# Kernel tuning notes

Measured on AMD Instinct MI355X. Metric: run time of the kernel, lower is better.

Reference implementation:

```python
import jax, jax.numpy as jnp
import numpy as np

D_MODEL = 1024
NUM_HEADS = 16
NUM_GROUPS = 4
HEAD_DIM = D_MODEL // NUM_HEADS
ROPE_BASE = 10000.0


def _rope_tables(seq_len, head_dim, dtype=jnp.float32):
    inv_freq = 1.0 / (ROPE_BASE ** (jnp.arange(0, head_dim, 2, dtype=jnp.float32) / head_dim))
    freqs = jnp.arange(seq_len, dtype=jnp.float32)[:, None] * inv_freq[None, :]  # [S, hd/2]
    emb = jnp.concatenate([freqs, freqs], axis=-1)  # [S, hd]
    return jnp.cos(emb).astype(dtype), jnp.sin(emb).astype(dtype)


def _rotate_half(t):
    half = t.shape[-1] // 2
    return jnp.concatenate([-t[..., half:], t[..., :half]], axis=-1)


def _apply_rope(t, cos, sin):
    # t: [B,S,H,hd]; cos/sin: [S,hd] broadcast over batch and heads
    c = cos[None, :, None, :]
    s = sin[None, :, None, :]
    return t * c + _rotate_half(t) * s


def setup_inputs() -> dict:
    key = jax.random.key(0)
    ks = jax.random.split(key, 5)
    B, S, D = 2, 2048, D_MODEL
    scale = 1.0 / np.sqrt(D)
    return {
        "x": jax.random.normal(ks[0], (B, S, D), dtype=jnp.float32),
        "Wq": jax.random.normal(ks[1], (D, D), dtype=jnp.float32) * scale,
        "Wk": jax.random.normal(ks[2], (D, D), dtype=jnp.float32) * scale,
        "Wv": jax.random.normal(ks[3], (D, D), dtype=jnp.float32) * scale,
        "Wo": jax.random.normal(ks[4], (D, D), dtype=jnp.float32) * scale,
    }


def reference(x, Wq, Wk, Wv, Wo):
    B, S, D = x.shape
    H, G, hd = NUM_HEADS, NUM_GROUPS, HEAD_DIM
    hpg = H // G  # heads per group

    q = (x @ Wq.T).reshape(B, S, H, hd)
    k = (x @ Wk.T).reshape(B, S, H, hd)
    v = (x @ Wv.T).reshape(B, S, H, hd)

    cos, sin = _rope_tables(S, hd, x.dtype)
    q = _apply_rope(q, cos, sin)
    k = _apply_rope(k, cos, sin)

    # query head reordering: [B,S,G,hpg,hd] -> transpose(2,3) -> [B,S,H,hd]
    q = q.reshape(B, S, G, hpg, hd).swapaxes(2, 3).reshape(B, S, H, hd)
    # GQA group-mean of K/V, then repeat back to H heads
    k = k.reshape(B, S, G, hpg, hd).mean(axis=3)  # [B,S,G,hd]
    v = v.reshape(B, S, G, hpg, hd).mean(axis=3)
    k = jnp.repeat(k, hpg, axis=2)  # [B,S,H,hd]
    v = jnp.repeat(v, hpg, axis=2)

    q = q.transpose(0, 2, 1, 3)  # [B,H,S,hd]
    k = k.transpose(0, 2, 1, 3)
    v = v.transpose(0, 2, 1, 3)

    scores = jnp.einsum('bhqd,bhkd->bhqk', q, k) / np.sqrt(hd)  # [B,H,S,S]
    probs = jax.nn.softmax(scores, axis=-1)
    attn = jnp.einsum('bhqk,bhkd->bhqd', probs, v)

    attn = attn.transpose(0, 2, 1, 3).reshape(B, S, D)
    return attn @ Wo.T
```

## Files before the change

### kernel.cpp

```cpp
#include <hip/hip_runtime.h>
#include <hip/hip_bf16.h>
#include <math.h>

#define B_ 2
#define S_ 2048
#define D_ 1024
#define H_ 16
#define G_ 4
#define HD_ 64

typedef float f32x4  __attribute__((ext_vector_type(4)));
typedef float f32x16 __attribute__((ext_vector_type(16)));
typedef short s16x8  __attribute__((ext_vector_type(8)));
typedef unsigned short u16x4 __attribute__((ext_vector_type(4)));
typedef unsigned int   u32x4 __attribute__((ext_vector_type(4)));

__device__ __forceinline__ unsigned short f2b(float f) {
    __hip_bfloat16 h = __float2bfloat16(f);
    return __builtin_bit_cast(unsigned short, h);
}
__device__ __forceinline__ unsigned cvtpk(float lo, float hi) {
    unsigned r;
    asm("v_cvt_pk_bf16_f32 %0, %1, %2" : "=v"(r) : "v"(lo), "v"(hi));
    return r;
}
__device__ __forceinline__ void plswap(unsigned &a, unsigned &b) {
    asm("v_permlane32_swap_b32 %0, %1" : "+v"(a), "+v"(b));
}

#define MFMA16(a, b, c) __builtin_amdgcn_mfma_f32_16x16x32_bf16(a, b, c, 0, 0, 0)
#define MFMA32(a, b, c) __builtin_amdgcn_mfma_f32_32x32x16_bf16(a, b, c, 0, 0, 0)

#define GLOAD16(gp, lp) __builtin_amdgcn_global_load_lds(                      \
    (const __attribute__((address_space(1))) void*)(gp),                      \
    (__attribute__((address_space(3))) void*)(lp), 16, 0, 0)

__global__ __launch_bounds__(256)
void prep_all(const float* __restrict__ x,  const float* __restrict__ Wq,
              const float* __restrict__ Wk, const float* __restrict__ Wv,
              const float* __restrict__ Wo,
              unsigned short* __restrict__ xb, unsigned short* __restrict__ wb,
              unsigned short* __restrict__ wob,
              float* __restrict__ cost, float* __restrict__ sint)
{
    const int NQ_WB = (1536*1024)/4;
    const int NQ_WO = (1024*1024)/4;
    const int NQ_X  = (B_*S_*D_)/4;
    int q = blockIdx.x*256 + threadIdx.x;
    if (q < NQ_WB) {
        const int idx = q*4, row = idx >> 10, c = idx & 1023;
        u16x4 o;
        if (row < 1024) {
            f32x4 v = *(const f32x4*)&Wq[(size_t)row*1024 + c];
            #pragma unroll
            for (int j = 0; j < 4; ++j) o[j] = f2b(v[j]);
        } else {
            const int rd = row - 1024, kv = rd >> 8, gd = rd & 255;
            const int g = gd >> 6, d = gd & 63;
            const float* W = kv ? Wv : Wk;
            f32x4 sum = {0.f, 0.f, 0.f, 0.f};
            #pragma unroll
            for (int p = 0; p < 4; ++p)
                sum += *(const f32x4*)&W[(size_t)((g*4 + p)*64 + d)*1024 + c];
            #pragma unroll
            for (int j = 0; j < 4; ++j) o[j] = f2b(sum[j]*0.25f);
        }
        *(u16x4*)&wb[idx] = o;
        return;
    }
    q -= NQ_WB;
    if (q < NQ_WO) {
        const int idx = q*4;
        f32x4 v = *(const f32x4*)&Wo[idx];
        u16x4 o;
        #pragma unroll
        for (int j = 0; j < 4; ++j) o[j] = f2b(v[j]);
        *(u16x4*)&wob[idx] = o;
        return;
    }
    q -= NQ_WO;
    if (q < NQ_X) {
        const int idx = q*4;
        f32x4 v = *(const f32x4*)&x[idx];
        u16x4 o;
        #pragma unroll
        for (int j = 0; j < 4; ++j) o[j] = f2b(v[j]);
        *(u16x4*)&xb[idx] = o;
        return;
    }
    q -= NQ_X;
    if (q < (S_*32)/4) {
        const int idx = q*4, s = idx >> 5, f0 = idx & 31;
        #pragma unroll
        for (int j = 0; j < 4; ++j) {
            const float f = (float)(f0 + j);
            const float fr = (float)s * powf(10000.0f, -f*(1.0f/32.0f));
            cost[idx + j] = cosf(fr);
            sint[idx + j] = sinf(fr);
        }
    }
}

template<int MODE>
__global__ __launch_bounds__(256)
void gemm_mfma(const unsigned short* __restrict__ Am,
               const unsigned short* __restrict__ Bm,
               unsigned short* __restrict__ qr,
               unsigned short* __restrict__ kr,
               unsigned short* __restrict__ vt,
               float* __restrict__ outf,
               const float* __restrict__ cost,
               const float* __restrict__ sint,
               int nbx)
{
    __shared__ unsigned short As[2][64*64];
    __shared__ unsigned short Bs[2][128*64];

    const int nwg = gridDim.x;
    const int cpx = nwg >> 3;
    const int bid = blockIdx.x;
    const int swz = (bid & 7)*cpx + (bid >> 3);
    const int bx = swz % nbx, by = swz / nbx;

    const int t  = threadIdx.x;
    const int w  = t >> 6, l = t & 63;
    const int lg = l >> 4, lr = l & 15;
    const int wr = w >> 1, wc = w & 1;

    const unsigned short* gA = Am + (size_t)by*64*D_;
    const unsigned short* gB = Bm + (size_t)bx*128*D_;

    const int srow = l >> 3;
    const int schk = (l & 7) ^ srow;

#define STAGE(buf, k0)                                                         \
    _Pragma("unroll")                                                          \
    for (int i_ = 0; i_ < 2; ++i_) {                                           \
        const int rowA_ = 16*w + 8*i_ + srow;                                  \
        GLOAD16(gA + (size_t)rowA_*D_ + (k0) + 8*schk, &As[buf][(16*w + 8*i_)*64]); \
    }                                                                          \
    _Pragma("unroll")                                                          \
    for (int i_ = 0; i_ < 4; ++i_) {                                           \
        const int rowB_ = 32*w + 8*i_ + srow;                                  \
        GLOAD16(gB + (size_t)rowB_*D_ + (k0) + 8*schk, &Bs[buf][(32*w + 8*i_)*64]); \
    }

    f32x4 acc[2][4] = {};

    STAGE(0, 0);
    #pragma unroll 1
    for (int kt = 0; kt < 16; ++kt) {
        const int cur = kt & 1;
        if (kt < 15) {
            STAGE(cur ^ 1, 64*(kt + 1));
            asm volatile("s_waitcnt vmcnt(6)" ::: "memory");
        } else {
            asm volatile("s_waitcnt vmcnt(0)" ::: "memory");
        }
        __builtin_amdgcn_s_barrier();

        #pragma unroll
        for (int kk = 0; kk < 2; ++kk) {
            s16x8 af[2], bfr[4];
            #pragma unroll
            for (int m = 0; m < 2; ++m) {
                const int row = 32*wr + 16*m + lr;
                af[m] = *(const s16x8*)&As[cur][row*64 + 8*((lg + 4*kk) ^ (row & 7))];
            }
            #pragma unroll
            for (int n = 0; n < 4; ++n) {
                const int col = 64*wc + 16*n + lr;
                bfr[n] = *(const s16x8*)&Bs[cur][col*64 + 8*((lg + 4*kk) ^ (col & 7))];
            }
            #pragma unroll
            for (int m = 0; m < 2; ++m)
                #pragma unroll
                for (int n = 0; n < 4; ++n)
                    acc[m][n] = MFMA16(af[m], bfr[n], acc[m][n]);
        }
        asm volatile("s_waitcnt lgkmcnt(0)" ::: "memory");
        __builtin_amdgcn_s_barrier();
    }
#undef STAGE

    if (MODE == 1) {
        #pragma unroll
        for (int m = 0; m < 2; ++m)
            #pragma unroll
            for (int r = 0; r < 4; ++r) {
                const int row = by*64 + 32*wr + 16*m + 4*lg + r;
                #pragma unroll
                for (int n = 0; n < 4; ++n)
                    outf[(size_t)row*D_ + bx*128 + 64*wc + 16*n + lr] = acc[m][n][r];
            }
        return;
    }

    if (bx < 10) {
        const float CQ = 0.18033688011112044f;
        #pragma unroll
        for (int m = 0; m < 2; ++m) {
            #pragma unroll
            for (int r = 0; r < 4; ++r) {
                const int row = by*64 + 32*wr + 16*m + 4*lg + r;
                const int b = row >> 11, s = row & (S_ - 1);
                const float c_lo = cost[s*32 + lr],      s_lo = sint[s*32 + lr];
                const float c_hi = cost[s*32 + 16 + lr], s_hi = sint[s*32 + 16 + lr];
                unsigned short vals[4];
                #pragma unroll
                for (int n = 0; n < 4; ++n) {
                    const float cc = (n & 1) ? c_hi : c_lo;
                    const float sn = (n & 1) ? s_hi : s_lo;
                    const float self = acc[m][n][r], part = acc[m][n ^ 2][r];
                    float rv = (n < 2) ? fmaf(self, cc, -part*sn)
                                       : fmaf(self, cc,  part*sn);
                    if (bx < 8) rv *= CQ;
                    vals[n] = f2b(rv);
                }
                size_t base;
                unsigned short* dst;
                if (bx < 8) {
                    const int hh = 2*bx + wc;
                    const int hp = (hh & 3)*4 + (hh >> 2);
                    base = (((size_t)b*H_ + hp)*S_ + s)*HD_;
                    dst = qr;
                } else {
                    const int g = (bx - 8)*2 + wc;
                    base = (((size_t)b*G_ + g)*S_ + s)*HD_;
                    dst = kr;
                }
                #pragma unroll
                for (int n = 0; n < 4; ++n) dst[base + 16*n + lr] = vals[n];
            }
        }
    } else {
        const int g = (bx - 10)*2 + wc;
        #pragma unroll
        for (int m = 0; m < 2; ++m) {
            const int row0 = by*64 + 32*wr + 16*m + 4*lg;
            const int b = row0 >> 11, s0 = row0 & (S_ - 1);
            #pragma unroll
            for (int n = 0; n < 4; ++n) {
                const int dd = 16*n + lr;
                u16x4 v;
                #pragma unroll
                for (int r = 0; r < 4; ++r) v[r] = f2b(acc[m][n][r]);
                *(u16x4*)&vt[(((size_t)b*G_ + g)*HD_ + dd)*S_ + s0] = v;
            }
        }
    }
}

__device__ __forceinline__ void stage64(const unsigned short* Kp, const unsigned short* Vp,
                                        unsigned short* ks, unsigned short* vs,
                                        int key0, int w, int l)
{
    const int srow = l >> 3;
    const int schk = (l & 7) ^ srow;
    #pragma unroll
    for (int i = 0; i < 2; ++i) {
        const int row = 16*w + 8*i + srow;
        GLOAD16(Kp + ((size_t)(key0 + row))*HD_ + 8*schk, ks + (16*w + 8*i)*64);
        GLOAD16(Vp + (size_t)row*S_ + key0 + 8*schk,      vs + (16*w + 8*i)*64);
    }
}

__global__ __launch_bounds__(512, 4)
void flash_attn_mfma(const unsigned short* __restrict__ qr,
                     const unsigned short* __restrict__ kr,
                     const unsigned short* __restrict__ vt,
                     unsigned short* __restrict__ attnb)
{
    __shared__ unsigned short Ks[2][2][64*64];
    __shared__ unsigned short Vs[2][2][64*64];

    const int bid  = blockIdx.x;
    const int cpx  = gridDim.x >> 3;
    const int swz  = (bid & 7)*cpx + (bid >> 3);
    const int qt   = swz & 15;
    const int h    = (swz >> 4) & 15;
    const int b    = swz >> 8;
    const int g    = h >> 2;
    const int t    = threadIdx.x;
    const int w8   = t >> 6;
    const int half = w8 >> 2;
    const int w    = w8 & 3;
    const int l    = t & 63;
    const int hi   = l >> 5;
    const int li   = l & 31;

    const unsigned short* Qp = qr + (((size_t)b*H_ + h)*S_ + (size_t)qt*128 + w*32)*HD_;
    const unsigned short* Kp = kr + ((size_t)b*G_ + g)*(size_t)S_*HD_ + (size_t)half*1024*HD_;
    const unsigned short* Vp = vt + ((size_t)b*G_ + g)*(size_t)HD_*S_ + half*1024;

    s16x8 qf[4];
    #pragma unroll
    for (int kk = 0; kk < 4; ++kk)
        qf[kk] = *(const s16x8*)(Qp + (size_t)li*HD_ + 16*kk + 8*hi);

    s16x8 ones;
    #pragma unroll
    for (int e = 0; e < 8; ++e) ones[e] = (short)0x3F80;

    f32x16 o[2], o_l;
    #pragma unroll
    for (int e = 0; e < 16; ++e) { o[0][e] = 0.f; o[1][e] = 0.f; o_l[e] = 0.f; }

    const int NT = 1024/64;
    stage64(Kp, Vp, Ks[half][0], Vs[half][0], 0, w, l);

    #pragma unroll 1
    for (int kt = 0; kt < NT; ++kt) {
        const int cur = kt & 1;
        if (kt + 1 < NT) {
            stage64(Kp, Vp, Ks[half][cur^1], Vs[half][cur^1], 64*(kt + 1), w, l);
            asm volatile("s_waitcnt vmcnt(4)" ::: "memory");
        } else {
            asm volatile("s_waitcnt vmcnt(0)" ::: "memory");
        }
        __builtin_amdgcn_s_barrier();

        f32x16 sc[2];
        #pragma unroll
        for (int q4 = 0; q4 < 2; ++q4)
            #pragma unroll
            for (int e = 0; e < 16; ++e) sc[q4][e] = 0.f;

        __builtin_amdgcn_s_setprio(1);
        #pragma unroll
        for (int kk = 0; kk < 4; ++kk) {
            const int chk = 8*((hi + 2*kk) ^ (li & 7));
            #pragma unroll
            for (int q4 = 0; q4 < 2; ++q4) {
                s16x8 kf = *(const s16x8*)&Ks[half][cur][(32*q4 + li)*64 + chk];
                sc[q4] = MFMA32(kf, qf[kk], sc[q4]);
            }
        }
        __builtin_amdgcn_s_setprio(0);

        #pragma unroll
        for (int q4 = 0; q4 < 2; ++q4)
            #pragma unroll
            for (int e = 0; e < 16; ++e)
                sc[q4][e] = __builtin_amdgcn_exp2f(sc[q4][e]);

        __builtin_amdgcn_s_setprio(1);
        #pragma unroll
        for (int q4 = 0; q4 < 2; ++q4) {
            #pragma unroll
            for (int s2 = 0; s2 < 2; ++s2) {
                unsigned a0 = cvtpk(sc[q4][8*s2+0], sc[q4][8*s2+1]);
                unsigned a1 = cvtpk(sc[q4][8*s2+2], sc[q4][8*s2+3]);
                unsigned a2 = cvtpk(sc[q4][8*s2+4], sc[q4][8*s2+5]);
                unsigned a3 = cvtpk(sc[q4][8*s2+6], sc[q4][8*s2+7]);
                plswap(a0, a2); plswap(a1, a3);
                u32x4 aw = {a0, a1, a2, a3};
                s16x8 paf = __builtin_bit_cast(s16x8, aw);
                const int ks = 2*q4 + s2;
                #pragma unroll
                for (int dt = 0; dt < 2; ++dt) {
                    const int d = li + 32*dt;
                    s16x8 vf = *(const s16x8*)&Vs[half][cur][d*64 + 8*((hi + 2*ks) ^ (li & 7))];
                    o[dt] = MFMA32(paf, vf, o[dt]);
                }
                o_l = MFMA32(paf, ones, o_l);
            }
        }
        __builtin_amdgcn_s_setprio(0);

        asm volatile("s_waitcnt lgkmcnt(0)" ::: "memory");
        __builtin_amdgcn_s_barrier();
    }

    float* ocomb = (float*)&Ks[0][0][0];
    float* lcomb = (float*)&Vs[0][0][0];
    __syncthreads();

    if (half == 1) {
        #pragma unroll
        for (int r = 0; r < 16; ++r) {
            const int qq  = (r & 3) + 8*(r >> 2) + 4*hi;
            const int row = w*32 + qq;
            ocomb[row*64 + li]      = o[0][r];
            ocomb[row*64 + li + 32] = o[1][r];
            if (li == 0) lcomb[row] = o_l[r];
        }
    }
    __syncthreads();
    if (half == 0) {
        #pragma unroll
        for (int r = 0; r < 16; ++r) {
            const int qq  = (r & 3) + 8*(r >> 2) + 4*hi;
            const int row = w*32 + qq;
            const int s   = qt*128 + row;
            const float inv = 1.0f / (o_l[r] + lcomb[row]);
            const float v0 = (o[0][r] + ocomb[row*64 + li])      * inv;
            const float v1 = (o[1][r] + ocomb[row*64 + li + 32]) * inv;
            attnb[((size_t)b*S_ + s)*D_ + h*HD_ + li]      = f2b(v0);
            attnb[((size_t)b*S_ + s)*D_ + h*HD_ + li + 32] = f2b(v1);
        }
    }
}

extern "C" void kernel_launch(void* const* d_in, const int* in_sizes, int n_in,
                              void* d_out, int out_size, void* d_ws, size_t ws_size,
                              hipStream_t stream)
{
    const float* x  = (const float*)d_in[0];
    const float* Wq = (const float*)d_in[1];
    const float* Wk = (const float*)d_in[2];
    const float* Wv = (const float*)d_in[3];
    const float* Wo = (const float*)d_in[4];
    float* out = (float*)d_out;

    char* p = (char*)d_ws;
    unsigned short* xb    = (unsigned short*)p; p += (size_t)B_*S_*D_*2;
    unsigned short* wb    = (unsigned short*)p; p += (size_t)1536*1024*2;
    unsigned short* wob   = (unsigned short*)p; p += (size_t)1024*1024*2;
    unsigned short* qr    = (unsigned short*)p; p += (size_t)B_*H_*S_*HD_*2;
    unsigned short* kr    = (unsigned short*)p; p += (size_t)B_*G_*S_*HD_*2;
    unsigned short* vt    = (unsigned short*)p; p += (size_t)B_*G_*HD_*S_*2;
    unsigned short* attnb = (unsigned short*)p; p += (size_t)B_*S_*D_*2;
    float* cost = (float*)p; p += (size_t)S_*32*4;
    float* sint = (float*)p;

    prep_all<<<6720, 256, 0, stream>>>(x, Wq, Wk, Wv, Wo, xb, wb, wob, cost, sint);
    gemm_mfma<0><<<64*12, 256, 0, stream>>>(xb, wb, qr, kr, vt, nullptr, cost, sint, 12);
    flash_attn_mfma<<<B_*H_*(S_/128), 512, 0, stream>>>(qr, kr, vt, attnb);
    gemm_mfma<1><<<64*8, 256, 0, stream>>>(attnb, wob, nullptr, nullptr, nullptr, out, cost, sint, 8);
}
```

Baseline: 99.13 us.

## Process both key halves within each wave instead of splitting across wave groups

The attention block shrinks from 512 to 256 threads. Each wave now processes both halves of the key range (A and B) itself, with separate accumulators, instead of two wave groups each taking one half and combining through shared memory. This removes the LDS cross-half reduction and its two block syncs at the end, and gives the scheduler two independent MFMA chains per wave. In exchange each wave holds twice the accumulator registers and does twice the LDS reads, and fewer waves per block may reduce latency hiding.

```diff
diff --git a/kernel.cpp b/kernel.cpp
--- a/kernel.cpp
+++ b/kernel.cpp
@@ -265,33 +265,35 @@
     }
 }
 
-__global__ __launch_bounds__(512, 4)
+__global__ __launch_bounds__(256, 2)
 void flash_attn_mfma(const unsigned short* __restrict__ qr,
                      const unsigned short* __restrict__ kr,
                      const unsigned short* __restrict__ vt,
                      unsigned short* __restrict__ attnb)
 {
-    __shared__ unsigned short Ks[2][2][64*64];
-    __shared__ unsigned short Vs[2][2][64*64];
-
-    const int bid  = blockIdx.x;
-    const int cpx  = gridDim.x >> 3;
-    const int swz  = (bid & 7)*cpx + (bid >> 3);
-    const int qt   = swz & 15;
-    const int h    = (swz >> 4) & 15;
-    const int b    = swz >> 8;
-    const int g    = h >> 2;
-    const int t    = threadIdx.x;
-    const int w8   = t >> 6;
-    const int half = w8 >> 2;
-    const int w    = w8 & 3;
-    const int l    = t & 63;
-    const int hi   = l >> 5;
-    const int li   = l & 31;
-
-    const unsigned short* Qp = qr + (((size_t)b*H_ + h)*S_ + (size_t)qt*128 + w*32)*HD_;
-    const unsigned short* Kp = kr + ((size_t)b*G_ + g)*(size_t)S_*HD_ + (size_t)half*1024*HD_;
-    const unsigned short* Vp = vt + ((size_t)b*G_ + g)*(size_t)HD_*S_ + half*1024;
+    __shared__ unsigned short KsA[2][64*64];
+    __shared__ unsigned short VsA[2][64*64];
+    __shared__ unsigned short KsB[2][64*64];
+    __shared__ unsigned short VsB[2][64*64];
+
+    const int bid = blockIdx.x;
+    const int cpx = gridDim.x >> 3;
+    const int swz = (bid & 7)*cpx + (bid >> 3);
+    const int qt  = swz & 15;
+    const int h   = (swz >> 4) & 15;
+    const int b   = swz >> 8;
+    const int g   = h >> 2;
+    const int t   = threadIdx.x;
+    const int w   = t >> 6;
+    const int l   = t & 63;
+    const int hi  = l >> 5;
+    const int li  = l & 31;
+
+    const unsigned short* Qp  = qr + (((size_t)b*H_ + h)*S_ + (size_t)qt*128 + w*32)*HD_;
+    const unsigned short* KpA = kr + ((size_t)b*G_ + g)*(size_t)S_*HD_;
+    const unsigned short* VpA = vt + ((size_t)b*G_ + g)*(size_t)HD_*S_;
+    const unsigned short* KpB = KpA + (size_t)1024*HD_;
+    const unsigned short* VpB = VpA + 1024;
 
     s16x8 qf[4];
     #pragma unroll
@@ -302,29 +304,34 @@
     #pragma unroll
     for (int e = 0; e < 8; ++e) ones[e] = (short)0x3F80;
 
-    f32x16 o[2], o_l;
+    f32x16 oA[2], oB[2], olA, olB;
     #pragma unroll
-    for (int e = 0; e < 16; ++e) { o[0][e] = 0.f; o[1][e] = 0.f; o_l[e] = 0.f; }
+    for (int e = 0; e < 16; ++e) {
+        oA[0][e] = 0.f; oA[1][e] = 0.f; olA[e] = 0.f;
+        oB[0][e] = 0.f; oB[1][e] = 0.f; olB[e] = 0.f;
+    }
 
     const int NT = 1024/64;
-    stage64(Kp, Vp, Ks[half][0], Vs[half][0], 0, w, l);
+    stage64(KpA, VpA, KsA[0], VsA[0], 0, w, l);
+    stage64(KpB, VpB, KsB[0], VsB[0], 0, w, l);
 
     #pragma unroll 1
     for (int kt = 0; kt < NT; ++kt) {
         const int cur = kt & 1;
         if (kt + 1 < NT) {
-            stage64(Kp, Vp, Ks[half][cur^1], Vs[half][cur^1], 64*(kt + 1), w, l);
-            asm volatile("s_waitcnt vmcnt(4)" ::: "memory");
+            stage64(KpA, VpA, KsA[cur^1], VsA[cur^1], 64*(kt + 1), w, l);
+            stage64(KpB, VpB, KsB[cur^1], VsB[cur^1], 64*(kt + 1), w, l);
+            asm volatile("s_waitcnt vmcnt(8)" ::: "memory");
         } else {
             asm volatile("s_waitcnt vmcnt(0)" ::: "memory");
         }
         __builtin_amdgcn_s_barrier();
 
-        f32x16 sc[2];
+        f32x16 scA[2], scB[2];
         #pragma unroll
         for (int q4 = 0; q4 < 2; ++q4)
             #pragma unroll
-            for (int e = 0; e < 16; ++e) sc[q4][e] = 0.f;
+            for (int e = 0; e < 16; ++e) { scA[q4][e] = 0.f; scB[q4][e] = 0.f; }
 
         __builtin_amdgcn_s_setprio(1);
         #pragma unroll
@@ -332,8 +339,17 @@
             const int chk = 8*((hi + 2*kk) ^ (li & 7));
             #pragma unroll
             for (int q4 = 0; q4 < 2; ++q4) {
-                s16x8 kf = *(const s16x8*)&Ks[half][cur][(32*q4 + li)*64 + chk];
-                sc[q4] = MFMA32(kf, qf[kk], sc[q4]);
+                s16x8 kfA = *(const s16x8*)&KsA[cur][(32*q4 + li)*64 + chk];
+                scA[q4] = MFMA32(kfA, qf[kk], scA[q4]);
+            }
+        }
+        #pragma unroll
+        for (int kk = 0; kk < 4; ++kk) {
+            const int chk = 8*((hi + 2*kk) ^ (li & 7));
+            #pragma unroll
+            for (int q4 = 0; q4 < 2; ++q4) {
+                s16x8 kfB = *(const s16x8*)&KsB[cur][(32*q4 + li)*64 + chk];
+                scB[q4] = MFMA32(kfB, qf[kk], scB[q4]);
             }
         }
         __builtin_amdgcn_s_setprio(0);
@@ -342,17 +358,17 @@
         for (int q4 = 0; q4 < 2; ++q4)
             #pragma unroll
             for (int e = 0; e < 16; ++e)
-                sc[q4][e] = __builtin_amdgcn_exp2f(sc[q4][e]);
+                scA[q4][e] = __builtin_amdgcn_exp2f(scA[q4][e]);
 
         __builtin_amdgcn_s_setprio(1);
         #pragma unroll
         for (int q4 = 0; q4 < 2; ++q4) {
             #pragma unroll
             for (int s2 = 0; s2 < 2; ++s2) {
-                unsigned a0 = cvtpk(sc[q4][8*s2+0], sc[q4][8*s2+1]);
-                unsigned a1 = cvtpk(sc[q4][8*s2+2], sc[q4][8*s2+3]);
-                unsigned a2 = cvtpk(sc[q4][8*s2+4], sc[q4][8*s2+5]);
-                unsigned a3 = cvtpk(sc[q4][8*s2+6], sc[q4][8*s2+7]);
+                unsigned a0 = cvtpk(scA[q4][8*s2+0], scA[q4][8*s2+1]);
+                unsigned a1 = cvtpk(scA[q4][8*s2+2], scA[q4][8*s2+3]);
+                unsigned a2 = cvtpk(scA[q4][8*s2+4], scA[q4][8*s2+5]);
+                unsigned a3 = cvtpk(scA[q4][8*s2+6], scA[q4][8*s2+7]);
                 plswap(a0, a2); plswap(a1, a3);
                 u32x4 aw = {a0, a1, a2, a3};
                 s16x8 paf = __builtin_bit_cast(s16x8, aw);
@@ -360,10 +376,40 @@
                 #pragma unroll
                 for (int dt = 0; dt < 2; ++dt) {
                     const int d = li + 32*dt;
-                    s16x8 vf = *(const s16x8*)&Vs[half][cur][d*64 + 8*((hi + 2*ks) ^ (li & 7))];
-                    o[dt] = MFMA32(paf, vf, o[dt]);
+                    s16x8 vf = *(const s16x8*)&VsA[cur][d*64 + 8*((hi + 2*ks) ^ (li & 7))];
+                    oA[dt] = MFMA32(paf, vf, oA[dt]);
                 }
-                o_l = MFMA32(paf, ones, o_l);
+                olA = MFMA32(paf, ones, olA);
+            }
+        }
+        __builtin_amdgcn_s_setprio(0);
+
+        #pragma unroll
+        for (int q4 = 0; q4 < 2; ++q4)
+            #pragma unroll
+            for (int e = 0; e < 16; ++e)
+                scB[q4][e] = __builtin_amdgcn_exp2f(scB[q4][e]);
+
+        __builtin_amdgcn_s_setprio(1);
+        #pragma unroll
+        for (int q4 = 0; q4 < 2; ++q4) {
+            #pragma unroll
+            for (int s2 = 0; s2 < 2; ++s2) {
+                unsigned b0 = cvtpk(scB[q4][8*s2+0], scB[q4][8*s2+1]);
+                unsigned b1 = cvtpk(scB[q4][8*s2+2], scB[q4][8*s2+3]);
+                unsigned b2 = cvtpk(scB[q4][8*s2+4], scB[q4][8*s2+5]);
+                unsigned b3 = cvtpk(scB[q4][8*s2+6], scB[q4][8*s2+7]);
+                plswap(b0, b2); plswap(b1, b3);
+                u32x4 bw = {b0, b1, b2, b3};
+                s16x8 pbf = __builtin_bit_cast(s16x8, bw);
+                const int ks = 2*q4 + s2;
+                #pragma unroll
+                for (int dt = 0; dt < 2; ++dt) {
+                    const int d = li + 32*dt;
+                    s16x8 vf = *(const s16x8*)&VsB[cur][d*64 + 8*((hi + 2*ks) ^ (li & 7))];
+                    oB[dt] = MFMA32(pbf, vf, oB[dt]);
+                }
+                olB = MFMA32(pbf, ones, olB);
             }
         }
         __builtin_amdgcn_s_setprio(0);
@@ -372,33 +418,15 @@
         __builtin_amdgcn_s_barrier();
     }
 
-    float* ocomb = (float*)&Ks[0][0][0];
-    float* lcomb = (float*)&Vs[0][0][0];
-    __syncthreads();
-
-    if (half == 1) {
-        #pragma unroll
-        for (int r = 0; r < 16; ++r) {
-            const int qq  = (r & 3) + 8*(r >> 2) + 4*hi;
-            const int row = w*32 + qq;
-            ocomb[row*64 + li]      = o[0][r];
-            ocomb[row*64 + li + 32] = o[1][r];
-            if (li == 0) lcomb[row] = o_l[r];
-        }
-    }
-    __syncthreads();
-    if (half == 0) {
-        #pragma unroll
-        for (int r = 0; r < 16; ++r) {
-            const int qq  = (r & 3) + 8*(r >> 2) + 4*hi;
-            const int row = w*32 + qq;
-            const int s   = qt*128 + row;
-            const float inv = 1.0f / (o_l[r] + lcomb[row]);
-            const float v0 = (o[0][r] + ocomb[row*64 + li])      * inv;
-            const float v1 = (o[1][r] + ocomb[row*64 + li + 32]) * inv;
-            attnb[((size_t)b*S_ + s)*D_ + h*HD_ + li]      = f2b(v0);
-            attnb[((size_t)b*S_ + s)*D_ + h*HD_ + li + 32] = f2b(v1);
-        }
+    #pragma unroll
+    for (int r = 0; r < 16; ++r) {
+        const int qq = (r & 3) + 8*(r >> 2) + 4*hi;
+        const int s  = qt*128 + w*32 + qq;
+        const float inv = 1.0f / (olA[r] + olB[r]);
+        #pragma unroll
+        for (int dt = 0; dt < 2; ++dt)
+            attnb[((size_t)b*S_ + s)*D_ + h*HD_ + li + 32*dt] =
+                f2b((oA[dt][r] + oB[dt][r]) * inv);
     }
 }
 
@@ -426,6 +454,6 @@
 
     prep_all<<<6720, 256, 0, stream>>>(x, Wq, Wk, Wv, Wo, xb, wb, wob, cost, sint);
     gemm_mfma<0><<<64*12, 256, 0, stream>>>(xb, wb, qr, kr, vt, nullptr, cost, sint, 12);
-    flash_attn_mfma<<<B_*H_*(S_/128), 512, 0, stream>>>(qr, kr, vt, attnb);
+    flash_attn_mfma<<<B_*H_*(S_/128), 256, 0, stream>>>(qr, kr, vt, attnb);
     gemm_mfma<1><<<64*8, 256, 0, stream>>>(attnb, wob, nullptr, nullptr, nullptr, out, cost, sint, 8);
 }
```

New measurement: 92.56 us. 6.6% less time.

## Give each attention wave two query fragments and sum row-sums before one MFMA

Applied to the files above, without the earlier changes.

The flash attention kernel drops from 8 waves to 4 per block, so each wave now covers 64 query rows as two 32-row fragments. Each K and V LDS fragment it reads feeds two MFMAs, which halves LDS read traffic per unit of work. The row-sum MFMA against a ones vector runs once per tile on pre-summed exp values rather than once per sub-block, so fewer MFMAs are issued. The pipeline also moves the prefetch after the barrier with a full vmcnt(0) wait and removes the trailing barrier, in exchange for more registers per wave and fewer waves to hide latency.

```diff
diff --git a/kernel.cpp b/kernel.cpp
--- a/kernel.cpp
+++ b/kernel.cpp
@@ -26,6 +26,15 @@
 }
 __device__ __forceinline__ void plswap(unsigned &a, unsigned &b) {
     asm("v_permlane32_swap_b32 %0, %1" : "+v"(a), "+v"(b));
+}
+__device__ __forceinline__ s16x8 pack8(const float* v) {
+    unsigned a0 = cvtpk(v[0], v[1]);
+    unsigned a1 = cvtpk(v[2], v[3]);
+    unsigned a2 = cvtpk(v[4], v[5]);
+    unsigned a3 = cvtpk(v[6], v[7]);
+    plswap(a0, a2); plswap(a1, a3);
+    u32x4 aw = {a0, a1, a2, a3};
+    return __builtin_bit_cast(s16x8, aw);
 }
 
 #define MFMA16(a, b, c) __builtin_amdgcn_mfma_f32_16x16x32_bf16(a, b, c, 0, 0, 0)
@@ -251,21 +260,7 @@
     }
 }
 
-__device__ __forceinline__ void stage64(const unsigned short* Kp, const unsigned short* Vp,
-                                        unsigned short* ks, unsigned short* vs,
-                                        int key0, int w, int l)
-{
-    const int srow = l >> 3;
-    const int schk = (l & 7) ^ srow;
-    #pragma unroll
-    for (int i = 0; i < 2; ++i) {
-        const int row = 16*w + 8*i + srow;
-        GLOAD16(Kp + ((size_t)(key0 + row))*HD_ + 8*schk, ks + (16*w + 8*i)*64);
-        GLOAD16(Vp + (size_t)row*S_ + key0 + 8*schk,      vs + (16*w + 8*i)*64);
-    }
-}
-
-__global__ __launch_bounds__(512, 4)
+__global__ __launch_bounds__(256, 2)
 void flash_attn_mfma(const unsigned short* __restrict__ qr,
                      const unsigned short* __restrict__ kr,
                      const unsigned short* __restrict__ vt,
@@ -283,94 +278,131 @@
     const int g    = h >> 2;
     const int t    = threadIdx.x;
     const int w8   = t >> 6;
-    const int half = w8 >> 2;
-    const int w    = w8 & 3;
+    const int half = w8 >> 1;
+    const int wi   = w8 & 1;
     const int l    = t & 63;
     const int hi   = l >> 5;
     const int li   = l & 31;
 
-    const unsigned short* Qp = qr + (((size_t)b*H_ + h)*S_ + (size_t)qt*128 + w*32)*HD_;
+    const unsigned short* Qp = qr + (((size_t)b*H_ + h)*S_ + (size_t)qt*128 + wi*64)*HD_;
     const unsigned short* Kp = kr + ((size_t)b*G_ + g)*(size_t)S_*HD_ + (size_t)half*1024*HD_;
     const unsigned short* Vp = vt + ((size_t)b*G_ + g)*(size_t)HD_*S_ + half*1024;
 
-    s16x8 qf[4];
+    s16x8 qf[2][4];
     #pragma unroll
-    for (int kk = 0; kk < 4; ++kk)
-        qf[kk] = *(const s16x8*)(Qp + (size_t)li*HD_ + 16*kk + 8*hi);
+    for (int f = 0; f < 2; ++f)
+        #pragma unroll
+        for (int kk = 0; kk < 4; ++kk)
+            qf[f][kk] = *(const s16x8*)(Qp + (size_t)(32*f + li)*HD_ + 16*kk + 8*hi);
 
     s16x8 ones;
     #pragma unroll
     for (int e = 0; e < 8; ++e) ones[e] = (short)0x3F80;
 
-    f32x16 o[2], o_l;
+    f32x16 zf;
     #pragma unroll
-    for (int e = 0; e < 16; ++e) { o[0][e] = 0.f; o[1][e] = 0.f; o_l[e] = 0.f; }
+    for (int e = 0; e < 16; ++e) zf[e] = 0.f;
+
+    f32x16 o[2][2], ol[2];
+    #pragma unroll
+    for (int f = 0; f < 2; ++f) {
+        #pragma unroll
+        for (int e = 0; e < 16; ++e) { o[f][0][e] = 0.f; o[f][1][e] = 0.f; ol[f][e] = 0.f; }
+    }
+
+    const int srow = l >> 3;
+    const int schk = (l & 7) ^ srow;
+
+#define STAGE(buf, key0)                                                       \
+    _Pragma("unroll")                                                          \
+    for (int i_ = 0; i_ < 4; ++i_) {                                           \
+        const int row_ = 32*wi + 8*i_ + srow;                                  \
+        GLOAD16(Kp + ((size_t)((key0) + row_))*HD_ + 8*schk,                   \
+                &Ks[half][buf][(32*wi + 8*i_)*64]);                            \
+        GLOAD16(Vp + (size_t)row_*S_ + (key0) + 8*schk,                        \
+                &Vs[half][buf][(32*wi + 8*i_)*64]);                            \
+    }
 
     const int NT = 1024/64;
-    stage64(Kp, Vp, Ks[half][0], Vs[half][0], 0, w, l);
+    STAGE(0, 0);
 
     #pragma unroll 1
     for (int kt = 0; kt < NT; ++kt) {
         const int cur = kt & 1;
-        if (kt + 1 < NT) {
-            stage64(Kp, Vp, Ks[half][cur^1], Vs[half][cur^1], 64*(kt + 1), w, l);
-            asm volatile("s_waitcnt vmcnt(4)" ::: "memory");
-        } else {
-            asm volatile("s_waitcnt vmcnt(0)" ::: "memory");
-        }
+        asm volatile("s_waitcnt vmcnt(0)" ::: "memory");
         __builtin_amdgcn_s_barrier();
-
-        f32x16 sc[2];
-        #pragma unroll
-        for (int q4 = 0; q4 < 2; ++q4)
-            #pragma unroll
-            for (int e = 0; e < 16; ++e) sc[q4][e] = 0.f;
-
+        if (kt + 1 < NT) { STAGE(cur ^ 1, 64*(kt + 1)); }
+
+        f32x16 sc[2][2];
         __builtin_amdgcn_s_setprio(1);
-        #pragma unroll
-        for (int kk = 0; kk < 4; ++kk) {
+        {
+            const int chk = 8*(hi ^ (li & 7));
+            s16x8 k0 = *(const s16x8*)&Ks[half][cur][(     li)*64 + chk];
+            s16x8 k1 = *(const s16x8*)&Ks[half][cur][(32 + li)*64 + chk];
+            sc[0][0] = MFMA32(k0, qf[0][0], zf);
+            sc[1][0] = MFMA32(k0, qf[1][0], zf);
+            sc[0][1] = MFMA32(k1, qf[0][0], zf);
+            sc[1][1] = MFMA32(k1, qf[1][0], zf);
+        }
+        #pragma unroll
+        for (int kk = 1; kk < 4; ++kk) {
             const int chk = 8*((hi + 2*kk) ^ (li & 7));
-            #pragma unroll
-            for (int q4 = 0; q4 < 2; ++q4) {
-                s16x8 kf = *(const s16x8*)&Ks[half][cur][(32*q4 + li)*64 + chk];
-                sc[q4] = MFMA32(kf, qf[kk], sc[q4]);
-            }
+            s16x8 k0 = *(const s16x8*)&Ks[half][cur][(     li)*64 + chk];
+            s16x8 k1 = *(const s16x8*)&Ks[half][cur][(32 + li)*64 + chk];
+            sc[0][0] = MFMA32(k0, qf[0][kk], sc[0][0]);
+            sc[1][0] = MFMA32(k0, qf[1][kk], sc[1][0]);
+            sc[0][1] = MFMA32(k1, qf[0][kk], sc[0][1]);
+            sc[1][1] = MFMA32(k1, qf[1][kk], sc[1][1]);
         }
         __builtin_amdgcn_s_setprio(0);
 
         #pragma unroll
-        for (int q4 = 0; q4 < 2; ++q4)
-            #pragma unroll
-            for (int e = 0; e < 16; ++e)
-                sc[q4][e] = __builtin_amdgcn_exp2f(sc[q4][e]);
+        for (int f = 0; f < 2; ++f)
+            #pragma unroll
+            for (int q4 = 0; q4 < 2; ++q4)
+                #pragma unroll
+                for (int e = 0; e < 16; ++e)
+                    sc[f][q4][e] = __builtin_amdgcn_exp2f(sc[f][q4][e]);
+
+        float ss0[8], ss1[8];
+        #pragma unroll
+        for (int j = 0; j < 8; ++j) {
+            ss0[j] = (sc[0][0][j] + sc[0][0][8+j]) + (sc[0][1][j] + sc[0][1][8+j]);
+            ss1[j] = (sc[1][0][j] + sc[1][0][8+j]) + (sc[1][1][j] + sc[1][1][8+j]);
+        }
 
         __builtin_amdgcn_s_setprio(1);
         #pragma unroll
         for (int q4 = 0; q4 < 2; ++q4) {
             #pragma unroll
             for (int s2 = 0; s2 < 2; ++s2) {
-                unsigned a0 = cvtpk(sc[q4][8*s2+0], sc[q4][8*s2+1]);
-                unsigned a1 = cvtpk(sc[q4][8*s2+2], sc[q4][8*s2+3]);
-                unsigned a2 = cvtpk(sc[q4][8*s2+4], sc[q4][8*s2+5]);
-                unsigned a3 = cvtpk(sc[q4][8*s2+6], sc[q4][8*s2+7]);
-                plswap(a0, a2); plswap(a1, a3);
-                u32x4 aw = {a0, a1, a2, a3};
-                s16x8 paf = __builtin_bit_cast(s16x8, aw);
-                const int ks = 2*q4 + s2;
+                float t0[8], t1[8];
+                #pragma unroll
+                for (int j = 0; j < 8; ++j) {
+                    t0[j] = sc[0][q4][8*s2 + j];
+                    t1[j] = sc[1][q4][8*s2 + j];
+                }
+                s16x8 pa0 = pack8(t0);
+                s16x8 pa1 = pack8(t1);
+                const int ks_ = 2*q4 + s2;
                 #pragma unroll
                 for (int dt = 0; dt < 2; ++dt) {
                     const int d = li + 32*dt;
-                    s16x8 vf = *(const s16x8*)&Vs[half][cur][d*64 + 8*((hi + 2*ks) ^ (li & 7))];
-                    o[dt] = MFMA32(paf, vf, o[dt]);
+                    s16x8 vf = *(const s16x8*)&Vs[half][cur][d*64 + 8*((hi + 2*ks_) ^ (li & 7))];
+                    o[0][dt] = MFMA32(pa0, vf, o[0][dt]);
+                    o[1][dt] = MFMA32(pa1, vf, o[1][dt]);
                 }
-                o_l = MFMA32(paf, ones, o_l);
-            }
+            }
+        }
+        {
+            s16x8 ps0 = pack8(ss0);
+            s16x8 ps1 = pack8(ss1);
+            ol[0] = MFMA32(ps0, ones, ol[0]);
+            ol[1] = MFMA32(ps1, ones, ol[1]);
         }
         __builtin_amdgcn_s_setprio(0);
-
-        asm volatile("s_waitcnt lgkmcnt(0)" ::: "memory");
-        __builtin_amdgcn_s_barrier();
-    }
+    }
+#undef STAGE
 
     float* ocomb = (float*)&Ks[0][0][0];
     float* lcomb = (float*)&Vs[0][0][0];
@@ -378,27 +410,32 @@
 
     if (half == 1) {
         #pragma unroll
-        for (int r = 0; r < 16; ++r) {
-            const int qq  = (r & 3) + 8*(r >> 2) + 4*hi;
-            const int row = w*32 + qq;
-            ocomb[row*64 + li]      = o[0][r];
-            ocomb[row*64 + li + 32] = o[1][r];
-            if (li == 0) lcomb[row] = o_l[r];
-        }
+        for (int f = 0; f < 2; ++f)
+            #pragma unroll
+            for (int r = 0; r < 16; ++r) {
+                const int qq  = (r & 3) + 8*(r >> 2) + 4*hi;
+                const int row = 64*wi + 32*f + qq;
+                ocomb[row*64 + li]      = o[f][0][r];
+                ocomb[row*64 + li + 32] = o[f][1][r];
+                if (li == 0) lcomb[row] = ol[f][r];
+            }
     }
     __syncthreads();
     if (half == 0) {
         #pragma unroll
-        for (int r = 0; r < 16; ++r) {
-            const int qq  = (r & 3) + 8*(r >> 2) + 4*hi;
-            const int row = w*32 + qq;
-            const int s   = qt*128 + row;
-            const float inv = 1.0f / (o_l[r] + lcomb[row]);
-            const float v0 = (o[0][r] + ocomb[row*64 + li])      * inv;
-            const float v1 = (o[1][r] + ocomb[row*64 + li + 32]) * inv;
-            attnb[((size_t)b*S_ + s)*D_ + h*HD_ + li]      = f2b(v0);
-            attnb[((size_t)b*S_ + s)*D_ + h*HD_ + li + 32] = f2b(v1);
-        }
+        for (int f = 0; f < 2; ++f)
+            #pragma unroll
+            for (int r = 0; r < 16; ++r) {
+                const int qq  = (r & 3) + 8*(r >> 2) + 4*hi;
+                const int row = 64*wi + 32*f + qq;
+                const int s   = qt*128 + row;
+                const float inv = 1.0f / (ol[f][r] + lcomb[row]);
+                #pragma unroll
+                for (int dt = 0; dt < 2; ++dt) {
+                    const float v = (o[f][dt][r] + ocomb[row*64 + li + 32*dt]) * inv;
+                    attnb[((size_t)b*S_ + s)*D_ + h*HD_ + li + 32*dt] = f2b(v);
+                }
+            }
     }
 }
 
@@ -426,6 +463,6 @@
 
     prep_all<<<6720, 256, 0, stream>>>(x, Wq, Wk, Wv, Wo, xb, wb, wob, cost, sint);
     gemm_mfma<0><<<64*12, 256, 0, stream>>>(xb, wb, qr, kr, vt, nullptr, cost, sint, 12);
-    flash_attn_mfma<<<B_*H_*(S_/128), 512, 0, stream>>>(qr, kr, vt, attnb);
+    flash_attn_mfma<<<B_*H_*(S_/128), 256, 0, stream>>>(qr, kr, vt, attnb);
     gemm_mfma<1><<<64*8, 256, 0, stream>>>(attnb, wob, nullptr, nullptr, nullptr, out, cost, sint, 8);
 }
```

After: 99.75 us. No clear change (+0.6%).
